# Kernel optimization log

Measured on AMD Instinct MI355X. Metric: run time of the kernel, lower is better.

## Reference

```python
import jax, jax.numpy as jnp
import numpy as np

B, T, D_MODEL = 2, 1024, 512
EXPAND = 2
D_INNER = D_MODEL * EXPAND
STATE = 16
K_CONV = 4


def setup_inputs() -> dict:
    key = jax.random.key(0)
    ks = jax.random.split(key, 10)
    sc = lambda k, shape: jax.random.normal(k, shape, jnp.float32) * 0.02
    return {
        "x": jax.random.normal(ks[0], (B, T, D_MODEL), jnp.float32),
        "ln_g": jnp.ones((D_MODEL,), jnp.float32),
        "ln_b": jnp.zeros((D_MODEL,), jnp.float32),
        "W_in": sc(ks[1], (2 * D_INNER, D_MODEL)),
        "conv_w": sc(ks[2], (D_INNER, 1, K_CONV)),
        "conv_b": jnp.zeros((D_INNER,), jnp.float32),
        "W_B": sc(ks[3], (STATE, D_INNER)),
        "W_C": sc(ks[4], (STATE, D_INNER)),
        "W_dt": sc(ks[5], (D_INNER, D_INNER)),
        "b_dt": jax.random.uniform(ks[6], (D_INNER,), jnp.float32, -4.0, -1.0),
        # log_A init: A_diag = -(n+1) from HiPPO, log(-A_diag) = log(n+1), broadcast over d_inner
        "log_A": jnp.broadcast_to(jnp.log(jnp.arange(1, STATE + 1, dtype=jnp.float32)), (D_INNER, STATE)),
        "W_out": sc(ks[7], (D_MODEL, D_INNER)),
    }


def _silu(v):
    return v * jax.nn.sigmoid(v)


def reference(x, ln_g, ln_b, W_in, conv_w, conv_b, W_B, W_C, W_dt, b_dt, log_A, W_out):
    residual = x
    # LayerNorm (biased variance, eps=1e-5)
    mu = x.mean(-1, keepdims=True)
    var = x.var(-1, keepdims=True)
    xn = (x - mu) * jax.lax.rsqrt(var + 1e-5) * ln_g + ln_b
    # input projection and gate split
    xz = xn @ W_in.T                      # (B,T,2*D_INNER)
    x_main, z = jnp.split(xz, 2, axis=-1)
    # depthwise causal conv1d (padding=3 then slice to T == left-pad 3)
    xc = jnp.transpose(x_main, (0, 2, 1))  # (B,D_INNER,T)
    xc = jax.lax.conv_general_dilated(
        xc, conv_w, window_strides=(1,), padding=[(K_CONV - 1, 0)],
        dimension_numbers=("NCH", "OIH", "NCH"), feature_group_count=D_INNER,
    ) + conv_b[None, :, None]
    x_main = _silu(jnp.transpose(xc, (0, 2, 1)))  # (B,T,D_INNER)
    # selective scan in fp32
    xf = x_main.astype(jnp.float32)
    Bt = xf @ W_B.T                        # (B,T,N)
    Ct = xf @ W_C.T                        # (B,T,N)
    dt = jax.nn.softplus(xf @ W_dt.T + b_dt)  # (B,T,D_INNER)
    A = -jnp.exp(log_A)                    # (D_INNER,N)
    dA = jnp.exp(A[None, None] * dt[..., None])              # (B,T,D_INNER,N)
    dBx = dt[..., None] * Bt[:, :, None, :] * xf[..., None]  # (B,T,D_INNER,N)

    def comb(c1, c2):
        a1, b1 = c1
        a2, b2 = c2
        return a1 * a2, a2 * b1 + b2

    _, h = jax.lax.associative_scan(comb, (dA, dBx), axis=1)  # h_t = dA_t*h_{t-1}+dBx_t
    y = (h * Ct[:, :, None, :]).sum(-1).astype(x.dtype)       # (B,T,D_INNER)
    out = (y * _silu(z)) @ W_out.T
    return residual + out
```

## Files before the change

kernel.cpp:

```cpp
#include <hip/hip_runtime.h>

#define T_SEQ 1024
#define DM 512
#define DI 1024
#define NS 16
#define NC 32
#define CL 32

typedef __attribute__((ext_vector_type(8))) short short8;
typedef __attribute__((ext_vector_type(4))) float f32x4;
typedef unsigned short u16;
typedef unsigned int u32;

__device__ inline float b2f(u16 u) {
    unsigned v = ((unsigned)u) << 16;
    return __builtin_bit_cast(float, v);
}
__device__ inline u16 f2b(float f) {
    unsigned u = __builtin_bit_cast(unsigned, f);
    u += 0x7fff + ((u >> 16) & 1);
    return (u16)(u >> 16);
}

__device__ inline void g2l16(const u16* g, const short* l) {
    __builtin_amdgcn_global_load_lds((const __attribute__((address_space(1))) u32*)g,
                                     (__attribute__((address_space(3))) u32*)l, 16, 0, 0);
}

template<int K> __device__ __forceinline__ void vmwait() {
    if constexpr (K == 0)  asm volatile("s_waitcnt vmcnt(0)" ::: "memory");
    else if constexpr (K == 4)  asm volatile("s_waitcnt vmcnt(4)" ::: "memory");
    else if constexpr (K == 8)  asm volatile("s_waitcnt vmcnt(8)" ::: "memory");
    else if constexpr (K == 12) asm volatile("s_waitcnt vmcnt(12)" ::: "memory");
}

__global__ __launch_bounds__(256) void prep_k(const float* __restrict__ Win, const float* __restrict__ Wdt,
                       const float* __restrict__ Wout, const float* __restrict__ Wb,
                       const float* __restrict__ Wc,
                       u16* __restrict__ oWin, u16* __restrict__ wCat, u16* __restrict__ oWout,
                       const float* __restrict__ x, const float* __restrict__ g,
                       const float* __restrict__ be, u16* __restrict__ xn) {
    if (blockIdx.x < 2624) {
        int i = blockIdx.x * 256 + threadIdx.x;
        const float* s; u16* d; int off;
        if (i < 262144)      { s = Win;  d = oWin;  off = i; }
        else if (i < 524288) { s = Wdt;  d = wCat;  off = i - 262144; }
        else if (i < 655360) { s = Wout; d = oWout; off = i - 524288; }
        else if (i < 659456) { s = Wb;   d = wCat + 1048576; off = i - 655360; }
        else if (i < 663552) { s = Wc;   d = wCat + 1064960; off = i - 659456; }
        else {
            u16* dz = wCat + 1081344 + (i - 663552) * 4;
            dz[0] = 0; dz[1] = 0; dz[2] = 0; dz[3] = 0;
            return;
        }
        float4 v = ((const float4*)s)[off];
        d[off * 4 + 0] = f2b(v.x);
        d[off * 4 + 1] = f2b(v.y);
        d[off * 4 + 2] = f2b(v.z);
        d[off * 4 + 3] = f2b(v.w);
        return;
    }
    int row = blockIdx.x - 2624, tid = threadIdx.x;
    float2 v = ((const float2*)(x + row * DM))[tid];
    float s = v.x + v.y, q = v.x * v.x + v.y * v.y;
    #pragma unroll
    for (int m = 1; m < 64; m <<= 1) { s += __shfl_xor(s, m); q += __shfl_xor(q, m); }
    __shared__ float ss[4], qq[4];
    if ((tid & 63) == 0) { ss[tid >> 6] = s; qq[tid >> 6] = q; }
    __syncthreads();
    s = ss[0] + ss[1] + ss[2] + ss[3];
    q = qq[0] + qq[1] + qq[2] + qq[3];
    float mu = s / DM;
    float var = q / DM - mu * mu;
    float rs = rsqrtf(var + 1e-5f);
    int c = tid * 2;
    xn[row * DM + c]     = f2b((v.x - mu) * rs * g[c] + be[c]);
    xn[row * DM + c + 1] = f2b((v.y - mu) * rs * g[c + 1] + be[c + 1]);
}

template<int NT, int EPI>
__global__ __launch_bounds__(256) void gemm_bt(int gx,
                                               const u16* __restrict__ A, int lda,
                                               const u16* __restrict__ Bw, int ldb,
                                               void* __restrict__ outp, int ldo,
                                               const float* __restrict__ extra,
                                               float* __restrict__ BtF, float* __restrict__ CtF) {
    constexpr int ASZ = 64 * 64;
    __shared__ short a_sh[5 * ASZ];
    __shared__ short b_sh[5 * ASZ];
    int nwg = gridDim.x, q8 = nwg >> 3;
    int l = (blockIdx.x & 7) * q8 + (blockIdx.x >> 3);
    int bx = l % gx, by = l / gx;
    int tid = threadIdx.x, w = tid >> 6, lane = tid & 63;
    int m0 = bx * 64, n0 = by * 64;
    int wr = (w >> 1) * 32, wc = (w & 1) * 32;
    int lr = lane & 15, kg = lane >> 4;
    f32x4 acc[2][2] = {};
    const u16* Abase = A + (size_t)m0 * lda;
    const u16* Bbase = Bw + (size_t)n0 * ldb;
    int lrow = lane >> 3;
    int cl = lane & 7;
    int sc = cl ^ lrow;

    auto stage = [&](int buf, int kt) {
        int k0 = kt * 64;
        #pragma unroll
        for (int qq2 = 0; qq2 < 2; ++qq2) {
            int rowbase = qq2 * 32 + w * 8;
            int row = rowbase + lrow;
            g2l16(Abase + (size_t)row * lda + k0 + sc * 8, a_sh + buf * ASZ + rowbase * 64);
            g2l16(Bbase + (size_t)row * ldb + k0 + sc * 8, b_sh + buf * ASZ + rowbase * 64);
        }
    };

    stage(0, 0); stage(1, 1); stage(2, 2); stage(3, 3);
    for (int t = 0; t < NT; ++t) {
        int rem = NT - 1 - t;
        if (rem >= 3) vmwait<12>();
        else if (rem == 2) vmwait<8>();
        else if (rem == 1) vmwait<4>();
        else vmwait<0>();
        __builtin_amdgcn_s_barrier();
        if (t + 4 < NT) stage((t + 4) % 5, t + 4);
        const short* as = a_sh + (t % 5) * ASZ;
        const short* bs = b_sh + (t % 5) * ASZ;
        int rs = lr & 7;
        #pragma unroll
        for (int kk = 0; kk < 2; ++kk) {
            short8 af[2], bfr[2];
            #pragma unroll
            for (int i = 0; i < 2; ++i) {
                int row = wr + i * 16 + lr;
                af[i] = *(const short8*)&as[row * 64 + ((kk * 4 + kg) ^ rs) * 8];
            }
            #pragma unroll
            for (int j = 0; j < 2; ++j) {
                int row = wc + j * 16 + lr;
                bfr[j] = *(const short8*)&bs[row * 64 + ((kk * 4 + kg) ^ rs) * 8];
            }
            #pragma unroll
            for (int i = 0; i < 2; ++i)
                #pragma unroll
                for (int j = 0; j < 2; ++j)
                    acc[i][j] = __builtin_amdgcn_mfma_f32_16x16x32_bf16(af[i], bfr[j], acc[i][j], 0, 0, 0);
        }
    }

    int rb = (lane >> 4) * 4, cc = lane & 15;
    #pragma unroll
    for (int i = 0; i < 2; ++i) {
        #pragma unroll
        for (int j = 0; j < 2; ++j) {
            #pragma unroll
            for (int r = 0; r < 4; ++r) {
                int row = m0 + wr + i * 16 + rb + r;
                int col = n0 + wc + j * 16 + cc;
                float v = acc[i][j][r];
                if (EPI == 0) {
                    ((u16*)outp)[(size_t)row * ldo + col] = f2b(v);
                } else if (EPI == 2) {
                    ((float*)outp)[(size_t)row * ldo + col] = v + extra[(size_t)row * ldo + col];
                } else {
                    if (col < 1024) {
                        float xx = v + extra[col];
                        float sp = (xx > 20.f) ? xx : log1pf(__expf(xx));
                        ((u16*)outp)[(size_t)row * ldo + col] = f2b(sp);
                    } else if (col < 1040) {
                        BtF[(size_t)row * NS + (col - 1024)] = v;
                    } else if (col < 1056) {
                        CtF[(size_t)row * NS + (col - 1040)] = v;
                    }
                }
            }
        }
    }
}

__global__ void conv_k(const u16* __restrict__ xz, const float* __restrict__ w,
                       const float* __restrict__ cb, u16* __restrict__ xf) {
    int idx = blockIdx.x * 256 + threadIdx.x;
    int d = idx & (DI - 1);
    int bt = idx >> 10;
    int t = bt & (T_SEQ - 1);
    float s = cb[d];
    #pragma unroll
    for (int i = 0; i < 4; ++i) {
        int tt = t - 3 + i;
        if (tt >= 0) s += w[d * 4 + i] * b2f(xz[(size_t)(bt - 3 + i) * 2048 + d]);
    }
    float sig = 1.f / (1.f + __expf(-s));
    xf[idx] = f2b(s * sig);
}

__global__ __launch_bounds__(256) void scanA(const u16* __restrict__ dt, const u16* __restrict__ xf,
                                             const float* __restrict__ Bt, const float* __restrict__ logA,
                                             float* __restrict__ Aprod, float* __restrict__ S) {
    int tid = threadIdx.x;
    int dblk = blockIdx.x & 3;
    int c = (blockIdx.x >> 2) & (NC - 1);
    int b = blockIdx.x >> 7;
    int d = dblk * 256 + tid;
    float Adn[NS], ap[NS], h[NS];
    #pragma unroll
    for (int j = 0; j < 4; ++j)
        *(float4*)&Adn[j * 4] = ((const float4*)(logA + (size_t)d * NS))[j];
    #pragma unroll
    for (int n = 0; n < NS; ++n) { Adn[n] = -__expf(Adn[n]); ap[n] = 1.f; h[n] = 0.f; }
    const u16* dtp = dt + ((size_t)b * T_SEQ + c * CL) * DI + d;
    const u16* xfp = xf + ((size_t)b * T_SEQ + c * CL) * DI + d;
    const float* Bp = Bt + ((size_t)b * T_SEQ + c * CL) * NS;
    #pragma unroll 8
    for (int i = 0; i < CL; ++i) {
        float dtv = b2f(dtp[(size_t)i * DI]);
        float xv  = b2f(xfp[(size_t)i * DI]);
        float ux = dtv * xv;
        float Bv[NS];
        #pragma unroll
        for (int j = 0; j < 4; ++j) *(float4*)&Bv[j * 4] = ((const float4*)(Bp + (size_t)i * NS))[j];
        #pragma unroll
        for (int n = 0; n < NS; ++n) {
            float dA = __expf(Adn[n] * dtv);
            h[n] = fmaf(dA, h[n], ux * Bv[n]);
            ap[n] *= dA;
        }
    }
    size_t o = ((((size_t)c * 2 + b) * DI) + d) * NS;
    #pragma unroll
    for (int j = 0; j < 4; ++j) {
        ((float4*)(Aprod + o))[j] = *(float4*)&ap[j * 4];
        ((float4*)(S + o))[j]     = *(float4*)&h[j * 4];
    }
}

__global__ __launch_bounds__(256) void scanB(const float* __restrict__ Aprod, const float* __restrict__ S,
                                             float* __restrict__ Hin) {
    int chain = blockIdx.x * 256 + threadIdx.x;
    float h = 0.f;
    #pragma unroll 8
    for (int c = 0; c < NC; ++c) {
        size_t o = (size_t)c * 32768 + chain;
        Hin[o] = h;
        h = fmaf(Aprod[o], h, S[o]);
    }
}

__global__ __launch_bounds__(256) void scanC(const u16* __restrict__ dt, const u16* __restrict__ xf,
                                             const float* __restrict__ Bt, const float* __restrict__ Ct,
                                             const float* __restrict__ logA, const float* __restrict__ Hin,
                                             const u16* __restrict__ xz, u16* __restrict__ ym) {
    int tid = threadIdx.x;
    int dblk = blockIdx.x & 3;
    int c = (blockIdx.x >> 2) & (NC - 1);
    int b = blockIdx.x >> 7;
    int d = dblk * 256 + tid;
    float Adn[NS], h[NS];
    #pragma unroll
    for (int j = 0; j < 4; ++j)
        *(float4*)&Adn[j * 4] = ((const float4*)(logA + (size_t)d * NS))[j];
    #pragma unroll
    for (int n = 0; n < NS; ++n) Adn[n] = -__expf(Adn[n]);
    size_t o = ((((size_t)c * 2 + b) * DI) + d) * NS;
    #pragma unroll
    for (int j = 0; j < 4; ++j) *(float4*)&h[j * 4] = ((const float4*)(Hin + o))[j];
    const u16* dtp = dt + ((size_t)b * T_SEQ + c * CL) * DI + d;
    const u16* xfp = xf + ((size_t)b * T_SEQ + c * CL) * DI + d;
    const float* Bp = Bt + ((size_t)b * T_SEQ + c * CL) * NS;
    const float* Cp = Ct + ((size_t)b * T_SEQ + c * CL) * NS;
    const u16* zp = xz + ((size_t)b * T_SEQ + c * CL) * 2048 + 1024 + d;
    u16* yp = ym + ((size_t)b * T_SEQ + c * CL) * DI + d;
    #pragma unroll 8
    for (int i = 0; i < CL; ++i) {
        float dtv = b2f(dtp[(size_t)i * DI]);
        float xv  = b2f(xfp[(size_t)i * DI]);
        float ux = dtv * xv;
        float Bv[NS], Cv[NS];
        #pragma unroll
        for (int j = 0; j < 4; ++j) {
            *(float4*)&Bv[j * 4] = ((const float4*)(Bp + (size_t)i * NS))[j];
            *(float4*)&Cv[j * 4] = ((const float4*)(Cp + (size_t)i * NS))[j];
        }
        float r = 0.f;
        #pragma unroll
        for (int n = 0; n < NS; ++n) {
            float dA = __expf(Adn[n] * dtv);
            h[n] = fmaf(dA, h[n], ux * Bv[n]);
            r = fmaf(h[n], Cv[n], r);
        }
        float zv = b2f(zp[(size_t)i * 2048]);
        float sz = zv / (1.f + __expf(-zv));
        yp[(size_t)i * DI] = f2b(r * sz);
    }
}

extern "C" void kernel_launch(void* const* d_in, const int* in_sizes, int n_in,
                              void* d_out, int out_size, void* d_ws, size_t ws_size,
                              hipStream_t stream) {
    const float* x     = (const float*)d_in[0];
    const float* ln_g  = (const float*)d_in[1];
    const float* ln_b  = (const float*)d_in[2];
    const float* W_in  = (const float*)d_in[3];
    const float* conv_w= (const float*)d_in[4];
    const float* conv_b= (const float*)d_in[5];
    const float* W_B   = (const float*)d_in[6];
    const float* W_C   = (const float*)d_in[7];
    const float* W_dt  = (const float*)d_in[8];
    const float* b_dt  = (const float*)d_in[9];
    const float* log_A = (const float*)d_in[10];
    const float* W_out = (const float*)d_in[11];

    char* ws = (char*)d_ws;
    u16* wInB  = (u16*)(ws + 0);
    u16* wCat  = (u16*)(ws + 2097152);
    u16* wOutB = (u16*)(ws + 4325376);
    u16* xnB   = (u16*)(ws + 5373952);
    u16* xzB   = (u16*)(ws + 7471104);
    u16* xfB   = (u16*)(ws + 15859712);
    u16* dtB   = (u16*)(ws + 20054016);
    float* BtF = (float*)(ws + 24248320);
    float* CtF = (float*)(ws + 24379392);
    u16* ymB   = (u16*)(ws + 24510464);
    float* ApF = (float*)(ws + 28704768);
    float* SF  = (float*)(ws + 32899072);
    float* HiF = (float*)(ws + 37093376);

    prep_k<<<4672, 256, 0, stream>>>(W_in, W_dt, W_out, W_B, W_C, wInB, wCat, wOutB,
                                     x, ln_g, ln_b, xnB);
    gemm_bt<8, 0><<<1024, 256, 0, stream>>>(32, xnB, 512, wInB, 512,
            (void*)xzB, 2048, nullptr, nullptr, nullptr);
    conv_k<<<8192, 256, 0, stream>>>(xzB, conv_w, conv_b, xfB);
    gemm_bt<16, 4><<<544, 256, 0, stream>>>(32, xfB, 1024, wCat, 1024,
            (void*)dtB, 1024, b_dt, BtF, CtF);
    scanA<<<256, 256, 0, stream>>>(dtB, xfB, BtF, log_A, ApF, SF);
    scanB<<<128, 256, 0, stream>>>(ApF, SF, HiF);
    scanC<<<256, 256, 0, stream>>>(dtB, xfB, BtF, CtF, log_A, HiF, xzB, ymB);
    gemm_bt<16, 2><<<256, 256, 0, stream>>>(32, ymB, 1024, wOutB, 1024,
            d_out, 512, x, nullptr, nullptr);
}
```

Before: 131.9 us.

## Enlarge GEMM tiles to 128x128 and split-K the output projection

The GEMM core moves from 64x64 to 128x128 block tiles, with each wave holding a 4x4 MFMA accumulator grid and a 4-stage LDS pipeline instead of 5. This cuts redundant global loads and raises MFMA density. The output projection, which would otherwise launch only 64 blocks, becomes a 4-way split-K over 256 blocks writing fp32 partials, and a separate merge kernel sums them with the residual. The cost is fewer blocks for the input and dt GEMMs (256 and 144), more register pressure, an extra launch, and extra partial-buffer traffic. The partials reuse scan scratch buffers plus one new workspace region.

After: 144.1 us. +9.2%, slower.

```diff
diff --git a/kernel.cpp b/kernel.cpp
--- a/kernel.cpp
+++ b/kernel.cpp
@@ -29,9 +29,8 @@
 
 template<int K> __device__ __forceinline__ void vmwait() {
     if constexpr (K == 0)  asm volatile("s_waitcnt vmcnt(0)" ::: "memory");
-    else if constexpr (K == 4)  asm volatile("s_waitcnt vmcnt(4)" ::: "memory");
     else if constexpr (K == 8)  asm volatile("s_waitcnt vmcnt(8)" ::: "memory");
-    else if constexpr (K == 12) asm volatile("s_waitcnt vmcnt(12)" ::: "memory");
+    else if constexpr (K == 16) asm volatile("s_waitcnt vmcnt(16)" ::: "memory");
 }
 
 __global__ __launch_bounds__(256) void prep_k(const float* __restrict__ Win, const float* __restrict__ Wdt,
@@ -79,23 +78,18 @@
 }
 
 template<int NT, int EPI>
-__global__ __launch_bounds__(256) void gemm_bt(int gx,
-                                               const u16* __restrict__ A, int lda,
-                                               const u16* __restrict__ Bw, int ldb,
-                                               void* __restrict__ outp, int ldo,
-                                               const float* __restrict__ extra,
-                                               float* __restrict__ BtF, float* __restrict__ CtF) {
-    constexpr int ASZ = 64 * 64;
-    __shared__ short a_sh[5 * ASZ];
-    __shared__ short b_sh[5 * ASZ];
-    int nwg = gridDim.x, q8 = nwg >> 3;
-    int l = (blockIdx.x & 7) * q8 + (blockIdx.x >> 3);
-    int bx = l % gx, by = l / gx;
+__device__ __forceinline__ void gemm_core(int bx, int by,
+        const u16* __restrict__ A, int lda, const u16* __restrict__ Bw, int ldb,
+        void* __restrict__ outp, int ldo, const float* __restrict__ extra,
+        float* __restrict__ BtF, float* __restrict__ CtF) {
+    constexpr int SSZ = 128 * 64;
+    __shared__ short a_sh[4 * SSZ];
+    __shared__ short b_sh[4 * SSZ];
     int tid = threadIdx.x, w = tid >> 6, lane = tid & 63;
-    int m0 = bx * 64, n0 = by * 64;
-    int wr = (w >> 1) * 32, wc = (w & 1) * 32;
+    int m0 = bx * 128, n0 = by * 128;
+    int wr = (w >> 1) * 64, wc = (w & 1) * 64;
     int lr = lane & 15, kg = lane >> 4;
-    f32x4 acc[2][2] = {};
+    f32x4 acc[4][4] = {};
     const u16* Abase = A + (size_t)m0 * lda;
     const u16* Bbase = Bw + (size_t)n0 * ldb;
     int lrow = lane >> 3;
@@ -105,52 +99,51 @@
     auto stage = [&](int buf, int kt) {
         int k0 = kt * 64;
         #pragma unroll
-        for (int qq2 = 0; qq2 < 2; ++qq2) {
-            int rowbase = qq2 * 32 + w * 8;
+        for (int q = 0; q < 4; ++q) {
+            int rowbase = q * 32 + w * 8;
             int row = rowbase + lrow;
-            g2l16(Abase + (size_t)row * lda + k0 + sc * 8, a_sh + buf * ASZ + rowbase * 64);
-            g2l16(Bbase + (size_t)row * ldb + k0 + sc * 8, b_sh + buf * ASZ + rowbase * 64);
+            g2l16(Abase + (size_t)row * lda + k0 + sc * 8, a_sh + buf * SSZ + rowbase * 64);
+            g2l16(Bbase + (size_t)row * ldb + k0 + sc * 8, b_sh + buf * SSZ + rowbase * 64);
         }
     };
 
-    stage(0, 0); stage(1, 1); stage(2, 2); stage(3, 3);
+    stage(0, 0); stage(1, 1); stage(2, 2);
     for (int t = 0; t < NT; ++t) {
         int rem = NT - 1 - t;
-        if (rem >= 3) vmwait<12>();
-        else if (rem == 2) vmwait<8>();
-        else if (rem == 1) vmwait<4>();
+        if (rem >= 2) vmwait<16>();
+        else if (rem == 1) vmwait<8>();
         else vmwait<0>();
         __builtin_amdgcn_s_barrier();
-        if (t + 4 < NT) stage((t + 4) % 5, t + 4);
-        const short* as = a_sh + (t % 5) * ASZ;
-        const short* bs = b_sh + (t % 5) * ASZ;
+        if (t + 3 < NT) stage((t + 3) & 3, t + 3);
+        const short* as = a_sh + (t & 3) * SSZ;
+        const short* bs = b_sh + (t & 3) * SSZ;
         int rs = lr & 7;
         #pragma unroll
         for (int kk = 0; kk < 2; ++kk) {
-            short8 af[2], bfr[2];
+            short8 af[4], bfr[4];
             #pragma unroll
-            for (int i = 0; i < 2; ++i) {
+            for (int i = 0; i < 4; ++i) {
                 int row = wr + i * 16 + lr;
                 af[i] = *(const short8*)&as[row * 64 + ((kk * 4 + kg) ^ rs) * 8];
             }
             #pragma unroll
-            for (int j = 0; j < 2; ++j) {
+            for (int j = 0; j < 4; ++j) {
                 int row = wc + j * 16 + lr;
                 bfr[j] = *(const short8*)&bs[row * 64 + ((kk * 4 + kg) ^ rs) * 8];
             }
             #pragma unroll
-            for (int i = 0; i < 2; ++i)
+            for (int i = 0; i < 4; ++i)
                 #pragma unroll
-                for (int j = 0; j < 2; ++j)
+                for (int j = 0; j < 4; ++j)
                     acc[i][j] = __builtin_amdgcn_mfma_f32_16x16x32_bf16(af[i], bfr[j], acc[i][j], 0, 0, 0);
         }
     }
 
     int rb = (lane >> 4) * 4, cc = lane & 15;
     #pragma unroll
-    for (int i = 0; i < 2; ++i) {
-        #pragma unroll
-        for (int j = 0; j < 2; ++j) {
+    for (int i = 0; i < 4; ++i) {
+        #pragma unroll
+        for (int j = 0; j < 4; ++j) {
             #pragma unroll
             for (int r = 0; r < 4; ++r) {
                 int row = m0 + wr + i * 16 + rb + r;
@@ -160,6 +153,8 @@
                     ((u16*)outp)[(size_t)row * ldo + col] = f2b(v);
                 } else if (EPI == 2) {
                     ((float*)outp)[(size_t)row * ldo + col] = v + extra[(size_t)row * ldo + col];
+                } else if (EPI == 3) {
+                    ((float*)outp)[(size_t)row * ldo + col] = v;
                 } else {
                     if (col < 1024) {
                         float xx = v + extra[col];
@@ -174,6 +169,50 @@
             }
         }
     }
+}
+
+__device__ __forceinline__ int xcd_swz() {
+    int nwg = gridDim.x;
+    return (blockIdx.x & 7) * (nwg >> 3) + (blockIdx.x >> 3);
+}
+
+template<int NT, int EPI>
+__global__ __launch_bounds__(256) void gemm_bt(int gx,
+                                               const u16* __restrict__ A, int lda,
+                                               const u16* __restrict__ Bw, int ldb,
+                                               void* __restrict__ outp, int ldo,
+                                               const float* __restrict__ extra,
+                                               float* __restrict__ BtF, float* __restrict__ CtF) {
+    int l = xcd_swz();
+    gemm_core<NT, EPI>(l % gx, l / gx, A, lda, Bw, ldb, outp, ldo, extra, BtF, CtF);
+}
+
+__global__ __launch_bounds__(256) void gemm2_k(const u16* __restrict__ ym, const u16* __restrict__ Wout,
+                                               float* __restrict__ p0, float* __restrict__ p1,
+                                               float* __restrict__ p2, float* __restrict__ p3) {
+    int l = xcd_swz();
+    int ks = l >> 6, rem = l & 63;
+    int bx = rem % 16, by = rem / 16;
+    float* p = (ks == 0) ? p0 : (ks == 1) ? p1 : (ks == 2) ? p2 : p3;
+    gemm_core<4, 3>(bx, by, ym + ks * 256, DI, Wout + ks * 256, DI,
+                    (void*)p, DM, nullptr, nullptr, nullptr);
+}
+
+__global__ __launch_bounds__(256) void merge_k(const float* __restrict__ p0, const float* __restrict__ p1,
+                                               const float* __restrict__ p2, const float* __restrict__ p3,
+                                               const float* __restrict__ x, float* __restrict__ out) {
+    int i = blockIdx.x * 256 + threadIdx.x;
+    float4 a = ((const float4*)p0)[i];
+    float4 b = ((const float4*)p1)[i];
+    float4 c = ((const float4*)p2)[i];
+    float4 d = ((const float4*)p3)[i];
+    float4 e = ((const float4*)x)[i];
+    float4 o;
+    o.x = a.x + b.x + c.x + d.x + e.x;
+    o.y = a.y + b.y + c.y + d.y + e.y;
+    o.z = a.z + b.z + c.z + d.z + e.z;
+    o.w = a.w + b.w + c.w + d.w + e.w;
+    ((float4*)out)[i] = o;
 }
 
 __global__ void conv_k(const u16* __restrict__ xz, const float* __restrict__ w,
@@ -322,17 +361,18 @@
     float* ApF = (float*)(ws + 28704768);
     float* SF  = (float*)(ws + 32899072);
     float* HiF = (float*)(ws + 37093376);
+    float* P3F = (float*)(ws + 41287680);
 
     prep_k<<<4672, 256, 0, stream>>>(W_in, W_dt, W_out, W_B, W_C, wInB, wCat, wOutB,
                                      x, ln_g, ln_b, xnB);
-    gemm_bt<8, 0><<<1024, 256, 0, stream>>>(32, xnB, 512, wInB, 512,
+    gemm_bt<8, 0><<<256, 256, 0, stream>>>(16, xnB, 512, wInB, 512,
             (void*)xzB, 2048, nullptr, nullptr, nullptr);
     conv_k<<<8192, 256, 0, stream>>>(xzB, conv_w, conv_b, xfB);
-    gemm_bt<16, 4><<<544, 256, 0, stream>>>(32, xfB, 1024, wCat, 1024,
+    gemm_bt<16, 4><<<144, 256, 0, stream>>>(16, xfB, 1024, wCat, 1024,
             (void*)dtB, 1024, b_dt, BtF, CtF);
     scanA<<<256, 256, 0, stream>>>(dtB, xfB, BtF, log_A, ApF, SF);
     scanB<<<128, 256, 0, stream>>>(ApF, SF, HiF);
     scanC<<<256, 256, 0, stream>>>(dtB, xfB, BtF, CtF, log_A, HiF, xzB, ymB);
-    gemm_bt<16, 2><<<256, 256, 0, stream>>>(32, ymB, 1024, wOutB, 1024,
-            d_out, 512, x, nullptr, nullptr);
-}
+    gemm2_k<<<256, 256, 0, stream>>>(ymB, wOutB, ApF, SF, HiF, P3F);
+    merge_k<<<1024, 256, 0, stream>>>(ApF, SF, HiF, P3F, x, (float*)d_out);
+}
```

## Use 8-wave 128x64 GEMM tiles with 3-stage pipeline and split-K output projection

Applied to the files above, without the earlier changes.

Replaces the 4-wave 64x64 GEMM with a 512-thread kernel that computes 128x64 tiles, cutting the LDS ring from 5 stages to 3 and adding s_setprio around the MFMA loop. The output projection is split into two K halves written to scratch buffers, then combined with the residual by a new elementwise merge kernel. The aim is more B-tile reuse and more blocks in flight for the small final GEMM. In exchange it adds an extra kernel launch, an extra round trip of fp32 partials through memory, and a shallower prefetch pipeline, and it drops the old block-order swizzle.

After: 113.5 us. 1.16x faster.

```diff
diff --git a/kernel.cpp b/kernel.cpp
--- a/kernel.cpp
+++ b/kernel.cpp
@@ -28,10 +28,8 @@
 }
 
 template<int K> __device__ __forceinline__ void vmwait() {
-    if constexpr (K == 0)  asm volatile("s_waitcnt vmcnt(0)" ::: "memory");
-    else if constexpr (K == 4)  asm volatile("s_waitcnt vmcnt(4)" ::: "memory");
-    else if constexpr (K == 8)  asm volatile("s_waitcnt vmcnt(8)" ::: "memory");
-    else if constexpr (K == 12) asm volatile("s_waitcnt vmcnt(12)" ::: "memory");
+    if constexpr (K == 0) asm volatile("s_waitcnt vmcnt(0)" ::: "memory");
+    else if constexpr (K == 3) asm volatile("s_waitcnt vmcnt(3)" ::: "memory");
 }
 
 __global__ __launch_bounds__(256) void prep_k(const float* __restrict__ Win, const float* __restrict__ Wdt,
@@ -79,20 +77,14 @@
 }
 
 template<int NT, int EPI>
-__global__ __launch_bounds__(256) void gemm_bt(int gx,
-                                               const u16* __restrict__ A, int lda,
-                                               const u16* __restrict__ Bw, int ldb,
-                                               void* __restrict__ outp, int ldo,
-                                               const float* __restrict__ extra,
-                                               float* __restrict__ BtF, float* __restrict__ CtF) {
-    constexpr int ASZ = 64 * 64;
-    __shared__ short a_sh[5 * ASZ];
-    __shared__ short b_sh[5 * ASZ];
-    int nwg = gridDim.x, q8 = nwg >> 3;
-    int l = (blockIdx.x & 7) * q8 + (blockIdx.x >> 3);
-    int bx = l % gx, by = l / gx;
+__device__ __forceinline__ void gemm_core8(int bx, int by,
+        const u16* __restrict__ A, int lda, const u16* __restrict__ Bw, int ldb,
+        void* __restrict__ outp, int ldo, const float* __restrict__ extra,
+        float* __restrict__ BtF, float* __restrict__ CtF) {
+    __shared__ short a_sh[3 * 8192];
+    __shared__ short b_sh[3 * 4096];
     int tid = threadIdx.x, w = tid >> 6, lane = tid & 63;
-    int m0 = bx * 64, n0 = by * 64;
+    int m0 = bx * 128, n0 = by * 64;
     int wr = (w >> 1) * 32, wc = (w & 1) * 32;
     int lr = lane & 15, kg = lane >> 4;
     f32x4 acc[2][2] = {};
@@ -100,43 +92,39 @@
     const u16* Bbase = Bw + (size_t)n0 * ldb;
     int lrow = lane >> 3;
     int cl = lane & 7;
-    int sc = cl ^ lrow;
+    int row1 = w * 8 + lrow;
+    int sc = cl ^ (row1 & 7);
 
     auto stage = [&](int buf, int kt) {
         int k0 = kt * 64;
-        #pragma unroll
-        for (int qq2 = 0; qq2 < 2; ++qq2) {
-            int rowbase = qq2 * 32 + w * 8;
-            int row = rowbase + lrow;
-            g2l16(Abase + (size_t)row * lda + k0 + sc * 8, a_sh + buf * ASZ + rowbase * 64);
-            g2l16(Bbase + (size_t)row * ldb + k0 + sc * 8, b_sh + buf * ASZ + rowbase * 64);
-        }
+        g2l16(Abase + (size_t)row1 * lda + k0 + sc * 8, a_sh + buf * 8192 + w * 512);
+        g2l16(Abase + (size_t)(row1 + 64) * lda + k0 + sc * 8, a_sh + buf * 8192 + 4096 + w * 512);
+        g2l16(Bbase + (size_t)row1 * ldb + k0 + sc * 8, b_sh + buf * 4096 + w * 512);
     };
 
-    stage(0, 0); stage(1, 1); stage(2, 2); stage(3, 3);
+    stage(0, 0);
+    stage(1, 1);
     for (int t = 0; t < NT; ++t) {
-        int rem = NT - 1 - t;
-        if (rem >= 3) vmwait<12>();
-        else if (rem == 2) vmwait<8>();
-        else if (rem == 1) vmwait<4>();
+        if (t + 1 < NT) vmwait<3>();
         else vmwait<0>();
         __builtin_amdgcn_s_barrier();
-        if (t + 4 < NT) stage((t + 4) % 5, t + 4);
-        const short* as = a_sh + (t % 5) * ASZ;
-        const short* bs = b_sh + (t % 5) * ASZ;
-        int rs = lr & 7;
+        if (t + 2 < NT) stage((t + 2) % 3, t + 2);
+        const short* as = a_sh + (t % 3) * 8192;
+        const short* bs = b_sh + (t % 3) * 4096;
+        int rsw = lr & 7;
+        __builtin_amdgcn_s_setprio(1);
         #pragma unroll
         for (int kk = 0; kk < 2; ++kk) {
             short8 af[2], bfr[2];
             #pragma unroll
             for (int i = 0; i < 2; ++i) {
                 int row = wr + i * 16 + lr;
-                af[i] = *(const short8*)&as[row * 64 + ((kk * 4 + kg) ^ rs) * 8];
+                af[i] = *(const short8*)&as[row * 64 + ((kk * 4 + kg) ^ rsw) * 8];
             }
             #pragma unroll
             for (int j = 0; j < 2; ++j) {
                 int row = wc + j * 16 + lr;
-                bfr[j] = *(const short8*)&bs[row * 64 + ((kk * 4 + kg) ^ rs) * 8];
+                bfr[j] = *(const short8*)&bs[row * 64 + ((kk * 4 + kg) ^ rsw) * 8];
             }
             #pragma unroll
             for (int i = 0; i < 2; ++i)
@@ -144,6 +132,7 @@
                 for (int j = 0; j < 2; ++j)
                     acc[i][j] = __builtin_amdgcn_mfma_f32_16x16x32_bf16(af[i], bfr[j], acc[i][j], 0, 0, 0);
         }
+        __builtin_amdgcn_s_setprio(0);
     }
 
     int rb = (lane >> 4) * 4, cc = lane & 15;
@@ -160,6 +149,8 @@
                     ((u16*)outp)[(size_t)row * ldo + col] = f2b(v);
                 } else if (EPI == 2) {
                     ((float*)outp)[(size_t)row * ldo + col] = v + extra[(size_t)row * ldo + col];
+                } else if (EPI == 3) {
+                    ((float*)outp)[(size_t)row * ldo + col] = v;
                 } else {
                     if (col < 1024) {
                         float xx = v + extra[col];
@@ -174,6 +165,41 @@
             }
         }
     }
+}
+
+template<int NT, int EPI>
+__global__ __launch_bounds__(512) void gemm8(int gx,
+                                             const u16* __restrict__ A, int lda,
+                                             const u16* __restrict__ Bw, int ldb,
+                                             void* __restrict__ outp, int ldo,
+                                             const float* __restrict__ extra,
+                                             float* __restrict__ BtF, float* __restrict__ CtF) {
+    int bx = blockIdx.x % gx, by = blockIdx.x / gx;
+    gemm_core8<NT, EPI>(bx, by, A, lda, Bw, ldb, outp, ldo, extra, BtF, CtF);
+}
+
+__global__ __launch_bounds__(512) void gemm2_k(const u16* __restrict__ ym, const u16* __restrict__ Wout,
+                                               float* __restrict__ p0, float* __restrict__ p1) {
+    int bid = blockIdx.x;
+    int h = bid >> 7, rem = bid & 127;
+    int bx = rem & 15, by = rem >> 4;
+    float* p = h ? p1 : p0;
+    gemm_core8<8, 3>(bx, by, ym + h * 512, DI, Wout + h * 512, DI,
+                     (void*)p, DM, nullptr, nullptr, nullptr);
+}
+
+__global__ __launch_bounds__(256) void merge_k(const float* __restrict__ p0, const float* __restrict__ p1,
+                                               const float* __restrict__ x, float* __restrict__ out) {
+    int i = blockIdx.x * 256 + threadIdx.x;
+    float4 a = ((const float4*)p0)[i];
+    float4 b = ((const float4*)p1)[i];
+    float4 e = ((const float4*)x)[i];
+    float4 o;
+    o.x = a.x + b.x + e.x;
+    o.y = a.y + b.y + e.y;
+    o.z = a.z + b.z + e.z;
+    o.w = a.w + b.w + e.w;
+    ((float4*)out)[i] = o;
 }
 
 __global__ void conv_k(const u16* __restrict__ xz, const float* __restrict__ w,
@@ -325,14 +351,14 @@
 
     prep_k<<<4672, 256, 0, stream>>>(W_in, W_dt, W_out, W_B, W_C, wInB, wCat, wOutB,
                                      x, ln_g, ln_b, xnB);
-    gemm_bt<8, 0><<<1024, 256, 0, stream>>>(32, xnB, 512, wInB, 512,
+    gemm8<8, 0><<<512, 512, 0, stream>>>(16, xnB, 512, wInB, 512,
             (void*)xzB, 2048, nullptr, nullptr, nullptr);
     conv_k<<<8192, 256, 0, stream>>>(xzB, conv_w, conv_b, xfB);
-    gemm_bt<16, 4><<<544, 256, 0, stream>>>(32, xfB, 1024, wCat, 1024,
+    gemm8<16, 4><<<272, 512, 0, stream>>>(16, xfB, 1024, wCat, 1024,
             (void*)dtB, 1024, b_dt, BtF, CtF);
     scanA<<<256, 256, 0, stream>>>(dtB, xfB, BtF, log_A, ApF, SF);
     scanB<<<128, 256, 0, stream>>>(ApF, SF, HiF);
     scanC<<<256, 256, 0, stream>>>(dtB, xfB, BtF, CtF, log_A, HiF, xzB, ymB);
-    gemm_bt<16, 2><<<256, 256, 0, stream>>>(32, ymB, 1024, wOutB, 1024,
-            d_out, 512, x, nullptr, nullptr);
-}
+    gemm2_k<<<256, 512, 0, stream>>>(ymB, wOutB, ApF, SF);
+    merge_k<<<1024, 256, 0, stream>>>(ApF, SF, x, (float*)d_out);
+}
```
